# Kernel optimization log

Measured on AMD Instinct MI355X. Metric: run time of the kernel, lower is better.

The kernel has to match this reference:

```python
import jax, jax.numpy as jnp
import numpy as np

B, T, DP, DQ, DO = 128, 2048, 256, 256, 256


def setup_inputs() -> dict:
    key = jax.random.key(0)
    ks = jax.random.split(key, 10)
    return {
        "input_p": jax.random.normal(ks[0], (B, DP), dtype=jnp.float32),
        "mask_p": jnp.ones((B,), dtype=jnp.float32),
        "input_q": jax.random.normal(ks[1], (B, T, DQ), dtype=jnp.float32),
        "mask_q": jax.random.randint(ks[2], (B, T), 0, 2, dtype=jnp.int32),
        "h_tm1": jax.random.normal(ks[3], (B, DO), dtype=jnp.float32),
        # layer-0 parameters (depth == 0)
        "W_p_r": jax.random.normal(ks[4], (DO, DP + DO), dtype=jnp.float32) * 0.04,
        "b_p_r": jnp.zeros((DO,), dtype=jnp.float32),
        "W_q": jax.random.normal(ks[5], (DO, DQ), dtype=jnp.float32) * 0.05,
        "b_q": jnp.zeros((DO,), dtype=jnp.float32),
        "w": jax.random.normal(ks[6], (DO,), dtype=jnp.float32) * 0.05,
        "match_b": jnp.ones((1,), dtype=jnp.float32),
        "depth": 0,
    }


def masked_softmax(x, m, axis=-1):
    x = jnp.clip(x, -15.0, 15.0)
    x = x * m
    e_x = jnp.exp(x - jnp.max(x, axis=axis, keepdims=True))
    e_x = e_x * m
    return e_x / (jnp.sum(e_x, axis=axis, keepdims=True) + 1e-6)


def reference(input_p, mask_p, input_q, mask_q, h_tm1, W_p_r, b_p_r, W_q, b_q, w, match_b, depth):
    mq = mask_q.astype(jnp.float32)
    # G_p_r: [B, 1, DO]
    G_p_r = (jnp.concatenate([input_p, h_tm1], axis=-1) @ W_p_r.T + b_p_r)[:, None, :]
    # G_q: [B, T, DO]
    G_q = input_q @ W_q.T + b_q
    G = jnp.tanh(G_p_r + G_q)
    alpha = jnp.einsum("btd,d->bt", G, w) + match_b  # [B, T]
    alpha = masked_softmax(alpha, mq, axis=-1)
    z = jnp.einsum("bt,btd->bd", alpha, input_q)  # bmm context
    return jnp.concatenate([input_p, z], axis=1)  # [B, DP+DQ]
```

## Files before the change

### kernel.cpp

```cpp
#include <hip/hip_runtime.h>
#include <hip/hip_bf16.h>

typedef short short8 __attribute__((ext_vector_type(8)));
typedef float floatx4 __attribute__((ext_vector_type(4)));

constexpr int Bn = 128, Tn = 2048, DPn = 256, DQn = 256, DOn = 256;
constexpr int NCH = Tn / 64;

__device__ inline unsigned pk2(float x, float y) {
    __hip_bfloat162 h = __float22bfloat162_rn(make_float2(x, y));
    return *(unsigned*)&h;
}
__device__ inline float fast_tanh(float x) {
    float e = __expf(2.0f * x);
    return 1.0f - 2.0f / (e + 1.0f);
}

__global__ __launch_bounds__(256) void cvt_wq_kernel(const float* __restrict__ wq,
                                                     unsigned short* __restrict__ wqbf) {
    int idx = blockIdx.x * 256 + threadIdx.x;
    float4 v = ((const float4*)wq)[idx];
    ((uint2*)wqbf)[idx] = make_uint2(pk2(v.x, v.y), pk2(v.z, v.w));
}

__global__ __launch_bounds__(256) void base_kernel(const float* __restrict__ input_p,
                                                   const float* __restrict__ h_tm1,
                                                   const float* __restrict__ Wpr,
                                                   const float* __restrict__ bpr,
                                                   const float* __restrict__ bq,
                                                   float* __restrict__ base) {
    __shared__ float v[512];
    int b = blockIdx.x, tid = threadIdx.x;
    v[tid]       = input_p[b * DPn + tid];
    v[256 + tid] = h_tm1[b * DOn + tid];
    __syncthreads();
    const float4* row = (const float4*)(Wpr + (size_t)tid * 512);
    const float4* vv  = (const float4*)v;
    float acc = 0.f;
#pragma unroll 8
    for (int i = 0; i < 128; i++) {
        float4 r = row[i], x = vv[i];
        acc = fmaf(r.x, x.x, acc);
        acc = fmaf(r.y, x.y, acc);
        acc = fmaf(r.z, x.z, acc);
        acc = fmaf(r.w, x.w, acc);
    }
    base[b * DOn + tid] = acc + bpr[tid] + bq[tid];
}

__global__ __launch_bounds__(256, 2) void fused_kernel(const float* __restrict__ q,
                                                       const unsigned short* __restrict__ wqbf,
                                                       const float* __restrict__ base,
                                                       const float* __restrict__ wvec,
                                                       const float* __restrict__ matchb,
                                                       const int* __restrict__ maskq,
                                                       float* __restrict__ zpart,
                                                       float* __restrict__ spart,
                                                       float* __restrict__ mpart) {
    __shared__ __align__(16) char shraw[32 * 64 * 16];
    unsigned short* qtile = (unsigned short*)shraw;
    __shared__ float partl[4][64];
    __shared__ float earr[64];

    int b = blockIdx.y, c = blockIdx.x;
    int t0 = c * 64;
    int tid = threadIdx.x;
    int w = tid >> 6, lane = tid & 63, l15 = lane & 15, quad = lane >> 4;

    short8 bfr[4][8];
    const unsigned short* bbase = wqbf + (size_t)(w * 64 + l15) * 256 + quad * 8;
#pragma unroll
    for (int nt = 0; nt < 4; nt++)
#pragma unroll
        for (int ks = 0; ks < 8; ks++)
            bfr[nt][ks] = *(const short8*)(bbase + nt * 16 * 256 + ks * 32);
    float bn[4], wn[4];
#pragma unroll
    for (int nt = 0; nt < 4; nt++) {
        int n = w * 64 + nt * 16 + l15;
        bn[nt] = base[b * DOn + n];
        wn[nt] = wvec[n];
    }

    {
        const float* src = q + ((size_t)b * Tn + t0 + w * 16 + l15) * DQn + quad * 8;
        unsigned short* dst = qtile + ((size_t)(w * 8) * 64 + lane) * 8;
#pragma unroll
        for (int ks = 0; ks < 8; ks++) {
            float4 v0 = *(const float4*)(src + ks * 32);
            float4 v1 = *(const float4*)(src + ks * 32 + 4);
            uint4 u;
            u.x = pk2(v0.x, v0.y);
            u.y = pk2(v0.z, v0.w);
            u.z = pk2(v1.x, v1.y);
            u.w = pk2(v1.z, v1.w);
            *(uint4*)(dst + ks * 512) = u;
        }
    }
    __syncthreads();

#pragma unroll
    for (int mt = 0; mt < 4; mt++) {
        short8 af[8];
        const unsigned short* ab = qtile + ((size_t)(mt * 8) * 64 + lane) * 8;
#pragma unroll
        for (int ks = 0; ks < 8; ks++) af[ks] = *(const short8*)(ab + ks * 512);
        float prow[4] = {0.f, 0.f, 0.f, 0.f};
#pragma unroll
        for (int nt = 0; nt < 4; nt++) {
            floatx4 acc = {0.f, 0.f, 0.f, 0.f};
#pragma unroll
            for (int ks = 0; ks < 8; ks++)
                acc = __builtin_amdgcn_mfma_f32_16x16x32_bf16(af[ks], bfr[nt][ks], acc, 0, 0, 0);
#pragma unroll
            for (int r = 0; r < 4; r++) {
                float g = fast_tanh(acc[r] + bn[nt]);
                prow[r] = fmaf(g, wn[nt], prow[r]);
            }
        }
#pragma unroll
        for (int off = 1; off < 16; off <<= 1)
#pragma unroll
            for (int r = 0; r < 4; r++) prow[r] += __shfl_xor(prow[r], off);
        if (l15 == 0) {
#pragma unroll
            for (int r = 0; r < 4; r++) partl[w][mt * 16 + quad * 4 + r] = prow[r];
        }
    }
    __syncthreads();

    if (tid < 64) {
        int t = tid;
        float lg = partl[0][t] + partl[1][t] + partl[2][t] + partl[3][t] + matchb[0];
        float m = (float)maskq[(size_t)b * Tn + t0 + t];
        float x = fminf(fmaxf(lg, -15.f), 15.f) * m;
        float e = __expf(x - 15.f) * m;
        earr[t] = e;
        float xm = x, es = e;
#pragma unroll
        for (int off = 1; off < 64; off <<= 1) {
            xm = fmaxf(xm, __shfl_xor(xm, off));
            es += __shfl_xor(es, off);
        }
        if (t == 0) {
            mpart[b * NCH + c] = xm;
            spart[b * NCH + c] = es;
        }
    }
    __syncthreads();

    {
        int o = lane & 31, h = lane >> 5, g = w * 2 + h;
        const float* qz = q + ((size_t)b * Tn + t0 + g * 8) * DQn + o * 8;
        float acc[8] = {0.f, 0.f, 0.f, 0.f, 0.f, 0.f, 0.f, 0.f};
#pragma unroll
        for (int s = 0; s < 8; s++) {
            float e = earr[g * 8 + s];
            float4 a0 = *(const float4*)(qz + (size_t)s * DQn);
            float4 a1 = *(const float4*)(qz + (size_t)s * DQn + 4);
            acc[0] = fmaf(e, a0.x, acc[0]);
            acc[1] = fmaf(e, a0.y, acc[1]);
            acc[2] = fmaf(e, a0.z, acc[2]);
            acc[3] = fmaf(e, a0.w, acc[3]);
            acc[4] = fmaf(e, a1.x, acc[4]);
            acc[5] = fmaf(e, a1.y, acc[5]);
            acc[6] = fmaf(e, a1.z, acc[6]);
            acc[7] = fmaf(e, a1.w, acc[7]);
        }
        float* zp = (float*)shraw;
        float* zrow = zp + g * 256 + o * 8;
        *(float4*)(zrow)     = make_float4(acc[0], acc[1], acc[2], acc[3]);
        *(float4*)(zrow + 4) = make_float4(acc[4], acc[5], acc[6], acc[7]);
    }
    __syncthreads();
    {
        const float* zp = (const float*)shraw;
        float zs = 0.f;
#pragma unroll
        for (int r = 0; r < 8; r++) zs += zp[r * 256 + tid];
        zpart[((size_t)b * NCH + c) * DQn + tid] = zs;
    }
}

__global__ __launch_bounds__(256) void final_kernel(const float* __restrict__ input_p,
                                                    const float* __restrict__ zpart,
                                                    const float* __restrict__ spart,
                                                    const float* __restrict__ mpart,
                                                    float* __restrict__ out) {
    int b = blockIdx.x, tid = threadIdx.x;
    float S = 0.f, mx = -1e30f;
#pragma unroll 8
    for (int c = 0; c < NCH; c++) {
        S += spart[b * NCH + c];
        mx = fmaxf(mx, mpart[b * NCH + c]);
    }
    float denom = S + 1e-6f * __expf(mx - 15.f);
    float inv = 1.0f / denom;
    float zs = 0.f;
#pragma unroll 8
    for (int c = 0; c < NCH; c++) zs += zpart[((size_t)b * NCH + c) * DQn + tid];
    out[(size_t)b * 512 + tid] = input_p[(size_t)b * DPn + tid];
    out[(size_t)b * 512 + 256 + tid] = zs * inv;
}

extern "C" void kernel_launch(void* const* d_in, const int* in_sizes, int n_in,
                              void* d_out, int out_size, void* d_ws, size_t ws_size,
                              hipStream_t stream) {
    const float* input_p = (const float*)d_in[0];
    const float* input_q = (const float*)d_in[2];
    const int*   mask_q  = (const int*)d_in[3];
    const float* h_tm1   = (const float*)d_in[4];
    const float* W_p_r   = (const float*)d_in[5];
    const float* b_p_r   = (const float*)d_in[6];
    const float* W_q     = (const float*)d_in[7];
    const float* b_q     = (const float*)d_in[8];
    const float* w       = (const float*)d_in[9];
    const float* match_b = (const float*)d_in[10];
    float* out = (float*)d_out;

    char* ws = (char*)d_ws;
    unsigned short* wqbf = (unsigned short*)ws;
    float* base  = (float*)(ws + 131072);
    float* zpart = (float*)(ws + 262144);
    float* spart = (float*)(ws + 262144 + 4194304);
    float* mpart = (float*)(ws + 262144 + 4194304 + 16384);

    cvt_wq_kernel<<<64, 256, 0, stream>>>(W_q, wqbf);
    base_kernel<<<Bn, 256, 0, stream>>>(input_p, h_tm1, W_p_r, b_p_r, b_q, base);
    fused_kernel<<<dim3(NCH, Bn), 256, 0, stream>>>(input_q, wqbf, base, w, match_b,
                                                    mask_q, zpart, spart, mpart);
    final_kernel<<<Bn, 256, 0, stream>>>(input_p, zpart, spart, mpart, out);
}
```

Measured before the change: 439.2 us.

## Make attention kernel persistent over sequence chunks with double-buffered q panels

Replaces the one-block-per-64-rows grid with 4 blocks per batch. Each block loops over 16 chunks of 32 rows, prefetching the next q rows into registers and a second LDS buffer while computing the current chunk. The W_q bf16 fragments are loaded into registers once per block instead of once per 64 rows. The weighted sum for z now reads the bf16 q tile already in LDS instead of re-reading fp32 q from global memory, which lowers precision. Softmax and z partials shrink from 32 to 4 per batch, which makes the final reduction cheaper but leaves fewer, longer-running blocks to fill the GPU.

Result: slower. 493.9 us (+12.5%).

```diff
diff --git a/kernel.cpp b/kernel.cpp
--- a/kernel.cpp
+++ b/kernel.cpp
@@ -5,11 +5,16 @@
 typedef float floatx4 __attribute__((ext_vector_type(4)));
 
 constexpr int Bn = 128, Tn = 2048, DPn = 256, DQn = 256, DOn = 256;
-constexpr int NCH = Tn / 64;
+constexpr int NPART = 4;
+constexpr int NITER = 16;
+constexpr int CR = 32;
 
 __device__ inline unsigned pk2(float x, float y) {
     __hip_bfloat162 h = __float22bfloat162_rn(make_float2(x, y));
     return *(unsigned*)&h;
+}
+__device__ inline float bf2f(unsigned short h) {
+    return __uint_as_float(((unsigned)h) << 16);
 }
 __device__ inline float fast_tanh(float x) {
     float e = __expf(2.0f * x);
@@ -48,24 +53,24 @@
     base[b * DOn + tid] = acc + bpr[tid] + bq[tid];
 }
 
-__global__ __launch_bounds__(256, 2) void fused_kernel(const float* __restrict__ q,
-                                                       const unsigned short* __restrict__ wqbf,
-                                                       const float* __restrict__ base,
-                                                       const float* __restrict__ wvec,
-                                                       const float* __restrict__ matchb,
-                                                       const int* __restrict__ maskq,
-                                                       float* __restrict__ zpart,
-                                                       float* __restrict__ spart,
-                                                       float* __restrict__ mpart) {
-    __shared__ __align__(16) char shraw[32 * 64 * 16];
-    unsigned short* qtile = (unsigned short*)shraw;
-    __shared__ float partl[4][64];
-    __shared__ float earr[64];
-
-    int b = blockIdx.y, c = blockIdx.x;
-    int t0 = c * 64;
-    int tid = threadIdx.x;
-    int w = tid >> 6, lane = tid & 63, l15 = lane & 15, quad = lane >> 4;
+__global__ __launch_bounds__(256, 2) void attn_kernel(const float* __restrict__ q,
+                                                      const unsigned short* __restrict__ wqbf,
+                                                      const float* __restrict__ base,
+                                                      const float* __restrict__ wvec,
+                                                      const float* __restrict__ matchb,
+                                                      const int* __restrict__ maskq,
+                                                      float* __restrict__ zpart,
+                                                      float* __restrict__ spart,
+                                                      float* __restrict__ mpart) {
+    __shared__ __align__(16) unsigned short panels[2][16][64][8];
+    __shared__ float partl[4][32];
+    __shared__ float earr[32];
+    __shared__ float zp[8][256];
+
+    int p = blockIdx.x, b = blockIdx.y;
+    int tid = threadIdx.x, w = tid >> 6, lane = tid & 63;
+    int l15 = lane & 15, quad = lane >> 4;
+    int tbase = p * (Tn / NPART);
 
     short8 bfr[4][8];
     const unsigned short* bbase = wqbf + (size_t)(w * 64 + l15) * 256 + quad * 8;
@@ -81,104 +86,141 @@
         bn[nt] = base[b * DOn + n];
         wn[nt] = wvec[n];
     }
-
+    float mb = matchb[0];
+
+    int c0 = lane & 7, rw = lane >> 3;
+    int srow = w * 8 + rw;
+    int smt = srow >> 4, ss = srow & 15;
+
+    int zo = tid & 31, zws = tid >> 5;
+
+    float zacc[8] = {0.f, 0.f, 0.f, 0.f, 0.f, 0.f, 0.f, 0.f};
+    float sacc = 0.f, macc = -1e30f;
+
+    float4 pf[8];
     {
-        const float* src = q + ((size_t)b * Tn + t0 + w * 16 + l15) * DQn + quad * 8;
-        unsigned short* dst = qtile + ((size_t)(w * 8) * 64 + lane) * 8;
-#pragma unroll
-        for (int ks = 0; ks < 8; ks++) {
-            float4 v0 = *(const float4*)(src + ks * 32);
-            float4 v1 = *(const float4*)(src + ks * 32 + 4);
+        const float4* qrow = (const float4*)(q + ((size_t)b * Tn + tbase + srow) * DQn);
+#pragma unroll
+        for (int k = 0; k < 4; k++) {
+            pf[2 * k]     = qrow[k * 16 + c0 * 2];
+            pf[2 * k + 1] = qrow[k * 16 + c0 * 2 + 1];
+        }
+#pragma unroll
+        for (int k = 0; k < 4; k++) {
+            int o = k * 8 + c0;
             uint4 u;
-            u.x = pk2(v0.x, v0.y);
-            u.y = pk2(v0.z, v0.w);
-            u.z = pk2(v1.x, v1.y);
-            u.w = pk2(v1.z, v1.w);
-            *(uint4*)(dst + ks * 512) = u;
-        }
-    }
-    __syncthreads();
-
-#pragma unroll
-    for (int mt = 0; mt < 4; mt++) {
-        short8 af[8];
-        const unsigned short* ab = qtile + ((size_t)(mt * 8) * 64 + lane) * 8;
-#pragma unroll
-        for (int ks = 0; ks < 8; ks++) af[ks] = *(const short8*)(ab + ks * 512);
-        float prow[4] = {0.f, 0.f, 0.f, 0.f};
-#pragma unroll
-        for (int nt = 0; nt < 4; nt++) {
-            floatx4 acc = {0.f, 0.f, 0.f, 0.f};
+            u.x = pk2(pf[2 * k].x, pf[2 * k].y);
+            u.y = pk2(pf[2 * k].z, pf[2 * k].w);
+            u.z = pk2(pf[2 * k + 1].x, pf[2 * k + 1].y);
+            u.w = pk2(pf[2 * k + 1].z, pf[2 * k + 1].w);
+            *(uint4*)&panels[0][smt * 8 + (o >> 2)][(o & 3) * 16 + ss][0] = u;
+        }
+    }
+
+    for (int it = 0; it < NITER; ++it) {
+        int cur = it & 1, nxt = cur ^ 1;
+        __syncthreads();
+
+        if (it + 1 < NITER) {
+            const float4* qrow =
+                (const float4*)(q + ((size_t)b * Tn + tbase + (it + 1) * CR + srow) * DQn);
+#pragma unroll
+            for (int k = 0; k < 4; k++) {
+                pf[2 * k]     = qrow[k * 16 + c0 * 2];
+                pf[2 * k + 1] = qrow[k * 16 + c0 * 2 + 1];
+            }
+        }
+
+#pragma unroll
+        for (int mt = 0; mt < 2; mt++) {
+            short8 af[8];
 #pragma unroll
             for (int ks = 0; ks < 8; ks++)
-                acc = __builtin_amdgcn_mfma_f32_16x16x32_bf16(af[ks], bfr[nt][ks], acc, 0, 0, 0);
-#pragma unroll
-            for (int r = 0; r < 4; r++) {
-                float g = fast_tanh(acc[r] + bn[nt]);
-                prow[r] = fmaf(g, wn[nt], prow[r]);
-            }
-        }
-#pragma unroll
-        for (int off = 1; off < 16; off <<= 1)
-#pragma unroll
-            for (int r = 0; r < 4; r++) prow[r] += __shfl_xor(prow[r], off);
-        if (l15 == 0) {
-#pragma unroll
-            for (int r = 0; r < 4; r++) partl[w][mt * 16 + quad * 4 + r] = prow[r];
-        }
-    }
-    __syncthreads();
-
-    if (tid < 64) {
-        int t = tid;
-        float lg = partl[0][t] + partl[1][t] + partl[2][t] + partl[3][t] + matchb[0];
-        float m = (float)maskq[(size_t)b * Tn + t0 + t];
-        float x = fminf(fmaxf(lg, -15.f), 15.f) * m;
-        float e = __expf(x - 15.f) * m;
-        earr[t] = e;
-        float xm = x, es = e;
-#pragma unroll
-        for (int off = 1; off < 64; off <<= 1) {
-            xm = fmaxf(xm, __shfl_xor(xm, off));
-            es += __shfl_xor(es, off);
-        }
-        if (t == 0) {
-            mpart[b * NCH + c] = xm;
-            spart[b * NCH + c] = es;
-        }
-    }
-    __syncthreads();
-
-    {
-        int o = lane & 31, h = lane >> 5, g = w * 2 + h;
-        const float* qz = q + ((size_t)b * Tn + t0 + g * 8) * DQn + o * 8;
-        float acc[8] = {0.f, 0.f, 0.f, 0.f, 0.f, 0.f, 0.f, 0.f};
-#pragma unroll
-        for (int s = 0; s < 8; s++) {
-            float e = earr[g * 8 + s];
-            float4 a0 = *(const float4*)(qz + (size_t)s * DQn);
-            float4 a1 = *(const float4*)(qz + (size_t)s * DQn + 4);
-            acc[0] = fmaf(e, a0.x, acc[0]);
-            acc[1] = fmaf(e, a0.y, acc[1]);
-            acc[2] = fmaf(e, a0.z, acc[2]);
-            acc[3] = fmaf(e, a0.w, acc[3]);
-            acc[4] = fmaf(e, a1.x, acc[4]);
-            acc[5] = fmaf(e, a1.y, acc[5]);
-            acc[6] = fmaf(e, a1.z, acc[6]);
-            acc[7] = fmaf(e, a1.w, acc[7]);
-        }
-        float* zp = (float*)shraw;
-        float* zrow = zp + g * 256 + o * 8;
-        *(float4*)(zrow)     = make_float4(acc[0], acc[1], acc[2], acc[3]);
-        *(float4*)(zrow + 4) = make_float4(acc[4], acc[5], acc[6], acc[7]);
-    }
+                af[ks] = *(const short8*)&panels[cur][mt * 8 + ks][quad * 16 + l15][0];
+            float prow[4] = {0.f, 0.f, 0.f, 0.f};
+#pragma unroll
+            for (int nt = 0; nt < 4; nt++) {
+                floatx4 acc = {0.f, 0.f, 0.f, 0.f};
+#pragma unroll
+                for (int ks = 0; ks < 8; ks++)
+                    acc = __builtin_amdgcn_mfma_f32_16x16x32_bf16(af[ks], bfr[nt][ks], acc, 0, 0, 0);
+#pragma unroll
+                for (int r = 0; r < 4; r++) {
+                    float g = fast_tanh(acc[r] + bn[nt]);
+                    prow[r] = fmaf(g, wn[nt], prow[r]);
+                }
+            }
+#pragma unroll
+            for (int off = 1; off < 16; off <<= 1)
+#pragma unroll
+                for (int r = 0; r < 4; r++) prow[r] += __shfl_xor(prow[r], off);
+            if (l15 == 0) {
+#pragma unroll
+                for (int r = 0; r < 4; r++) partl[w][mt * 16 + quad * 4 + r] = prow[r];
+            }
+        }
+        __syncthreads();
+
+        if (tid < CR) {
+            float lg = partl[0][tid] + partl[1][tid] + partl[2][tid] + partl[3][tid] + mb;
+            float m = (float)maskq[(size_t)b * Tn + tbase + it * CR + tid];
+            float x = fminf(fmaxf(lg, -15.f), 15.f) * m;
+            float e = __expf(x - 15.f) * m;
+            earr[tid] = e;
+            sacc += e;
+            macc = fmaxf(macc, x);
+        }
+        __syncthreads();
+
+#pragma unroll
+        for (int j = 0; j < 4; j++) {
+            int row = zws * 4 + ((j + zo) & 3);
+            int mt = row >> 4, s = row & 15;
+            short8 f = *(const short8*)&panels[cur][mt * 8 + (zo >> 2)][(zo & 3) * 16 + s][0];
+            float e = earr[row];
+#pragma unroll
+            for (int x = 0; x < 8; x++)
+                zacc[x] = fmaf(e, bf2f((unsigned short)f[x]), zacc[x]);
+        }
+
+        if (it + 1 < NITER) {
+#pragma unroll
+            for (int k = 0; k < 4; k++) {
+                int o = k * 8 + c0;
+                uint4 u;
+                u.x = pk2(pf[2 * k].x, pf[2 * k].y);
+                u.y = pk2(pf[2 * k].z, pf[2 * k].w);
+                u.z = pk2(pf[2 * k + 1].x, pf[2 * k + 1].y);
+                u.w = pk2(pf[2 * k + 1].z, pf[2 * k + 1].w);
+                *(uint4*)&panels[nxt][smt * 8 + (o >> 2)][(o & 3) * 16 + ss][0] = u;
+            }
+        }
+    }
+
     __syncthreads();
     {
-        const float* zp = (const float*)shraw;
+        float* zr = &zp[zws][zo * 8];
+        *(float4*)(zr)     = make_float4(zacc[0], zacc[1], zacc[2], zacc[3]);
+        *(float4*)(zr + 4) = make_float4(zacc[4], zacc[5], zacc[6], zacc[7]);
+    }
+    __syncthreads();
+    {
         float zs = 0.f;
 #pragma unroll
-        for (int r = 0; r < 8; r++) zs += zp[r * 256 + tid];
-        zpart[((size_t)b * NCH + c) * DQn + tid] = zs;
+        for (int g = 0; g < 8; g++) zs += zp[g][tid];
+        zpart[((size_t)b * NPART + p) * DQn + tid] = zs;
+    }
+    if (tid < CR) {
+        float S = sacc, M = macc;
+#pragma unroll
+        for (int off = 1; off < 32; off <<= 1) {
+            S += __shfl_xor(S, off);
+            M = fmaxf(M, __shfl_xor(M, off));
+        }
+        if (tid == 0) {
+            spart[b * NPART + p] = S;
+            mpart[b * NPART + p] = M;
+        }
     }
 }
 
@@ -189,16 +231,15 @@
                                                     float* __restrict__ out) {
     int b = blockIdx.x, tid = threadIdx.x;
     float S = 0.f, mx = -1e30f;
-#pragma unroll 8
-    for (int c = 0; c < NCH; c++) {
-        S += spart[b * NCH + c];
-        mx = fmaxf(mx, mpart[b * NCH + c]);
-    }
-    float denom = S + 1e-6f * __expf(mx - 15.f);
-    float inv = 1.0f / denom;
+#pragma unroll
+    for (int c = 0; c < NPART; c++) {
+        S += spart[b * NPART + c];
+        mx = fmaxf(mx, mpart[b * NPART + c]);
+    }
+    float inv = 1.0f / (S + 1e-6f * __expf(mx - 15.f));
     float zs = 0.f;
-#pragma unroll 8
-    for (int c = 0; c < NCH; c++) zs += zpart[((size_t)b * NCH + c) * DQn + tid];
+#pragma unroll
+    for (int c = 0; c < NPART; c++) zs += zpart[((size_t)b * NPART + c) * DQn + tid];
     out[(size_t)b * 512 + tid] = input_p[(size_t)b * DPn + tid];
     out[(size_t)b * 512 + 256 + tid] = zs * inv;
 }
@@ -222,12 +263,12 @@
     unsigned short* wqbf = (unsigned short*)ws;
     float* base  = (float*)(ws + 131072);
     float* zpart = (float*)(ws + 262144);
-    float* spart = (float*)(ws + 262144 + 4194304);
-    float* mpart = (float*)(ws + 262144 + 4194304 + 16384);
+    float* spart = (float*)(ws + 262144 + 524288);
+    float* mpart = (float*)(ws + 262144 + 524288 + 8192);
 
     cvt_wq_kernel<<<64, 256, 0, stream>>>(W_q, wqbf);
     base_kernel<<<Bn, 256, 0, stream>>>(input_p, h_tm1, W_p_r, b_p_r, b_q, base);
-    fused_kernel<<<dim3(NCH, Bn), 256, 0, stream>>>(input_q, wqbf, base, w, match_b,
-                                                    mask_q, zpart, spart, mpart);
+    attn_kernel<<<dim3(NPART, Bn), 256, 0, stream>>>(input_q, wqbf, base, w, match_b,
+                                                     mask_q, zpart, spart, mpart);
     final_kernel<<<Bn, 256, 0, stream>>>(input_p, zpart, spart, mpart, out);
 }
```
